# Optimization experiments

Hardware: AMD Instinct MI355X
Metric: run time of the kernel (lower is better)

## Reference

```python
import jax, jax.numpy as jnp
import numpy as np

N = 1048576
C = 128

def setup_inputs() -> dict:
    key = jax.random.key(0)
    k1, k2 = jax.random.split(key)
    # probabilities must be positive for log; uniform in (1e-6, 1)
    predicts = jax.random.uniform(k1, (N, C), dtype=jnp.float32, minval=1e-6, maxval=1.0)
    labels = jax.random.randint(k2, (N,), 0, C, dtype=jnp.int64)
    return {"predicts": predicts, "labels": labels}

def reference(predicts, labels):
    # loss = -(1/N) * sum_i log(predicts[i, labels[i]])
    labels = labels.reshape(-1)
    picked = jnp.take_along_axis(predicts, labels[:, None], axis=1)[:, 0]  # [N]
    return -jnp.mean(jnp.log(picked))
```

## Files before the change

### kernel.cpp

```cpp
#include <hip/hip_runtime.h>

#define BLOCK 256
#define PER_THREAD 8
#define C 128

__global__ __launch_bounds__(BLOCK) void ce_partial_kernel(
    const float* __restrict__ predicts,
    const int* __restrict__ labels,
    float* __restrict__ partial,
    int n)
{
    const int tid = blockIdx.x * BLOCK + threadIdx.x;
    const int i0 = tid * PER_THREAD;

    float s = 0.0f;
    if (i0 + PER_THREAD <= n) {
        int4 la = *reinterpret_cast<const int4*>(labels + i0);
        int4 lb = *reinterpret_cast<const int4*>(labels + i0 + 4);
        const float* row = predicts + (size_t)i0 * C;
        float p0 = row[0 * C + la.x];
        float p1 = row[1 * C + la.y];
        float p2 = row[2 * C + la.z];
        float p3 = row[3 * C + la.w];
        float p4 = row[4 * C + lb.x];
        float p5 = row[5 * C + lb.y];
        float p6 = row[6 * C + lb.z];
        float p7 = row[7 * C + lb.w];
        s = (__logf(p0) + __logf(p1)) + (__logf(p2) + __logf(p3)) +
            (__logf(p4) + __logf(p5)) + (__logf(p6) + __logf(p7));
    } else {
        for (int i = i0; i < n; ++i)
            s += __logf(predicts[(size_t)i * C + labels[i]]);
    }

    #pragma unroll
    for (int off = 32; off > 0; off >>= 1)
        s += __shfl_down(s, off, 64);

    __shared__ float wave_sums[BLOCK / 64];
    const int lane = threadIdx.x & 63;
    const int wv   = threadIdx.x >> 6;
    if (lane == 0) wave_sums[wv] = s;
    __syncthreads();

    if (threadIdx.x == 0) {
        partial[blockIdx.x] =
            wave_sums[0] + wave_sums[1] + wave_sums[2] + wave_sums[3];
    }
}

__global__ __launch_bounds__(256) void ce_final_kernel(
    const float* __restrict__ partial, int nparts,
    float neg_inv_n, float* __restrict__ out)
{
    float s = 0.0f;
    for (int i = threadIdx.x; i < nparts; i += 256)
        s += partial[i];

    #pragma unroll
    for (int off = 32; off > 0; off >>= 1)
        s += __shfl_down(s, off, 64);

    __shared__ float wave_sums[4];
    const int lane = threadIdx.x & 63;
    const int wv   = threadIdx.x >> 6;
    if (lane == 0) wave_sums[wv] = s;
    __syncthreads();

    if (threadIdx.x == 0) {
        float total = wave_sums[0] + wave_sums[1] + wave_sums[2] + wave_sums[3];
        out[0] = total * neg_inv_n;
    }
}

extern "C" void kernel_launch(void* const* d_in, const int* in_sizes, int n_in,
                              void* d_out, int out_size, void* d_ws, size_t ws_size,
                              hipStream_t stream) {
    const float* predicts = (const float*)d_in[0];
    const int*   labels   = (const int*)d_in[1];
    float*       out      = (float*)d_out;
    float*       partial  = (float*)d_ws;
    const int n = in_sizes[1];

    const int per_block = BLOCK * PER_THREAD;
    const int grid = (n + per_block - 1) / per_block;

    ce_partial_kernel<<<grid, BLOCK, 0, stream>>>(predicts, labels, partial, n);
    ce_final_kernel<<<1, 256, 0, stream>>>(partial, grid, -1.0f / (float)n, out);
}
```

Before: 598.6 us.

## Stream full rows coalesced instead of gathering one element per row

Replaces the per-thread scattered gather of one label-selected float per row with a block-wide coalesced float4 stream over every row. Labels are staged in LDS and each lane keeps only the element whose segment matches the label. This reads the whole predicts matrix, several times more bytes than the gather touches, in exchange for fully coalesced wide loads. The aim is to remove the latency-bound, uncoalesced gather pattern.

```diff
diff --git a/kernel.cpp b/kernel.cpp
--- a/kernel.cpp
+++ b/kernel.cpp
@@ -1,36 +1,42 @@
 #include <hip/hip_runtime.h>
 
 #define BLOCK 256
-#define PER_THREAD 8
+#define ROWS_PER_BLOCK 256
 #define C 128
+#define SEGS 32
 
-__global__ __launch_bounds__(BLOCK) void ce_partial_kernel(
+__global__ __launch_bounds__(BLOCK) void ce_stream_kernel(
     const float* __restrict__ predicts,
     const int* __restrict__ labels,
     float* __restrict__ partial,
     int n)
 {
-    const int tid = blockIdx.x * BLOCK + threadIdx.x;
-    const int i0 = tid * PER_THREAD;
+    __shared__ int lds_lab[ROWS_PER_BLOCK];
+    const int row0 = blockIdx.x * ROWS_PER_BLOCK;
+
+    {
+        const int g = row0 + threadIdx.x;
+        lds_lab[threadIdx.x] = (g < n) ? labels[g] : 0;
+    }
+    __syncthreads();
 
     float s = 0.0f;
-    if (i0 + PER_THREAD <= n) {
-        int4 la = *reinterpret_cast<const int4*>(labels + i0);
-        int4 lb = *reinterpret_cast<const int4*>(labels + i0 + 4);
-        const float* row = predicts + (size_t)i0 * C;
-        float p0 = row[0 * C + la.x];
-        float p1 = row[1 * C + la.y];
-        float p2 = row[2 * C + la.z];
-        float p3 = row[3 * C + la.w];
-        float p4 = row[4 * C + lb.x];
-        float p5 = row[5 * C + lb.y];
-        float p6 = row[6 * C + lb.z];
-        float p7 = row[7 * C + lb.w];
-        s = (__logf(p0) + __logf(p1)) + (__logf(p2) + __logf(p3)) +
-            (__logf(p4) + __logf(p5)) + (__logf(p6) + __logf(p7));
-    } else {
-        for (int i = i0; i < n; ++i)
-            s += __logf(predicts[(size_t)i * C + labels[i]]);
+    #pragma unroll 8
+    for (int j = 0; j < (ROWS_PER_BLOCK * SEGS) / BLOCK; ++j) {
+        const int f = j * BLOCK + threadIdx.x;
+        const int row_local = f >> 5;
+        const int seg = f & 31;
+        const int g = row0 + row_local;
+        if (g < n) {
+            const float4 p = *reinterpret_cast<const float4*>(
+                predicts + (size_t)g * C + seg * 4);
+            const int lab = lds_lab[row_local];
+            if ((lab >> 2) == seg) {
+                const float v = (lab & 2) ? ((lab & 1) ? p.w : p.z)
+                                          : ((lab & 1) ? p.y : p.x);
+                s += __logf(v);
+            }
+        }
     }
 
     #pragma unroll
@@ -68,8 +74,8 @@
     __syncthreads();
 
     if (threadIdx.x == 0) {
-        float total = wave_sums[0] + wave_sums[1] + wave_sums[2] + wave_sums[3];
-        out[0] = total * neg_inv_n;
+        out[0] = (wave_sums[0] + wave_sums[1] + wave_sums[2] + wave_sums[3])
+                 * neg_inv_n;
     }
 }
 
@@ -82,9 +88,8 @@
     float*       partial  = (float*)d_ws;
     const int n = in_sizes[1];
 
-    const int per_block = BLOCK * PER_THREAD;
-    const int grid = (n + per_block - 1) / per_block;
+    const int grid = (n + ROWS_PER_BLOCK - 1) / ROWS_PER_BLOCK;
 
-    ce_partial_kernel<<<grid, BLOCK, 0, stream>>>(predicts, labels, partial, n);
+    ce_stream_kernel<<<grid, BLOCK, 0, stream>>>(predicts, labels, partial, n);
     ce_final_kernel<<<1, 256, 0, stream>>>(partial, grid, -1.0f / (float)n, out);
 }
```

After: 615.4 us. 1.03x slower.
